# Optimization experiments

Hardware: AMD Instinct MI355X
Metric: run time of the kernel (lower is better)

Reference implementation:

```python
import jax, jax.numpy as jnp
import numpy as np

HIDDEN_SIZE = 1024
NUM_EXPERTS = 8
MOE_INTERMEDIATE_SIZE = 1408
NUM_EXPERTS_PER_TOK = 2
SHARED_EXPERT_INTERMEDIATE_SIZE = 2816
B, T = 2, 1024
W_SCALE = 0.02  # keep pre-activations in a sane range


def setup_inputs() -> dict:
    key = jax.random.key(0)
    ks = jax.random.split(key, 8)
    H, E, I, SI = HIDDEN_SIZE, NUM_EXPERTS, MOE_INTERMEDIATE_SIZE, SHARED_EXPERT_INTERMEDIATE_SIZE
    return {
        "x": jax.random.normal(ks[0], (B, T, H), jnp.float32),
        "gate_w": jax.random.normal(ks[1], (E, H), jnp.float32) * W_SCALE,
        "experts_gate_up": jax.random.normal(ks[2], (E, 2 * I, H), jnp.float32) * W_SCALE,
        "experts_down": jax.random.normal(ks[3], (E, H, I), jnp.float32) * W_SCALE,
        "shared_gate_w": jax.random.normal(ks[4], (SI, H), jnp.float32) * W_SCALE,
        "shared_up_w": jax.random.normal(ks[5], (SI, H), jnp.float32) * W_SCALE,
        "shared_down_w": jax.random.normal(ks[6], (H, SI), jnp.float32) * W_SCALE,
        "shared_expert_gate_w": jax.random.normal(ks[7], (1, H), jnp.float32) * W_SCALE,
    }


def reference(x, gate_w, experts_gate_up, experts_down,
              shared_gate_w, shared_up_w, shared_down_w, shared_expert_gate_w):
    Bx, Tx, H = x.shape
    E = gate_w.shape[0]
    I = experts_down.shape[2]
    x_flat = x.reshape(Bx * Tx, H)            # [N,H]

    # router
    logits = x_flat @ gate_w.T                # [N,E]
    scores = jax.nn.softmax(logits, axis=-1)  # [N,E]
    _, topk_ids = jax.lax.top_k(scores, NUM_EXPERTS_PER_TOK)  # [N,K]
    # NOTE: original normalizes topk_scores but never uses them; combine weight
    # is the RAW softmax score, zeroed for non-selected experts.
    in_topk = jax.nn.one_hot(topk_ids, E, dtype=x.dtype).sum(axis=1)  # [N,E] in {0,1}
    w = scores * in_topk                      # [N,E]

    # dense dispatch over all experts (combine weight zeros out non-routed)
    gu = jnp.einsum('nh,eih->nei', x_flat, experts_gate_up)  # [N,E,2I]
    g, u = gu[..., :I], gu[..., I:]
    h = jax.nn.silu(g) * u                    # [N,E,I]
    expert_out = jnp.einsum('nei,ehi->neh', h, experts_down)  # [N,E,H]
    out = jnp.einsum('neh,ne->nh', expert_out, w)              # [N,H]

    # shared expert (SwiGLU) with sigmoid gate
    shared = (jax.nn.silu(x_flat @ shared_gate_w.T) * (x_flat @ shared_up_w.T)) @ shared_down_w.T
    shared_weight = jax.nn.sigmoid(x_flat @ shared_expert_gate_w.T)  # [N,1]
    out = out + shared_weight * shared
    return out.reshape(Bx, Tx, H)
```

## Files before the change

### kernel.cpp

```cpp
#include <hip/hip_runtime.h>
#include <hip/hip_bf16.h>

#define H_DIM 1024
#define NE 8
#define IDIM 1408
#define SIDIM 2816
#define NTOK 2048

typedef __attribute__((ext_vector_type(8))) _Float16 half8;
typedef __attribute__((ext_vector_type(4))) float f32x4;

__global__ __launch_bounds__(256) void cvt_kernel(const float* __restrict__ src,
                                                  _Float16* __restrict__ dst) {
    size_t i = ((size_t)blockIdx.x * 256 + threadIdx.x) * 8;
    float4 a = *(const float4*)(src + i);
    float4 b = *(const float4*)(src + i + 4);
    half8 o;
    o[0] = (_Float16)a.x; o[1] = (_Float16)a.y; o[2] = (_Float16)a.z; o[3] = (_Float16)a.w;
    o[4] = (_Float16)b.x; o[5] = (_Float16)b.y; o[6] = (_Float16)b.z; o[7] = (_Float16)b.w;
    *(half8*)(dst + i) = o;
}

__global__ __launch_bounds__(256) void router_kernel(
    const float* __restrict__ x, const float* __restrict__ gate_w,
    const float* __restrict__ seg_w, float* __restrict__ wbuf,
    float* __restrict__ swbuf) {
    const int wave = threadIdx.x >> 6, lane = threadIdx.x & 63;
    const int n = blockIdx.x * 4 + wave;
    const float* xr = x + (size_t)n * H_DIM;
    float4 xv[4];
#pragma unroll
    for (int i = 0; i < 4; ++i) xv[i] = *(const float4*)(xr + i * 256 + lane * 4);
    float logits[9];
    for (int e = 0; e < 9; ++e) {
        const float* wr = (e < 8) ? (gate_w + (size_t)e * H_DIM) : seg_w;
        float p = 0.f;
#pragma unroll
        for (int i = 0; i < 4; ++i) {
            float4 wv = *(const float4*)(wr + i * 256 + lane * 4);
            p += xv[i].x * wv.x + xv[i].y * wv.y + xv[i].z * wv.z + xv[i].w * wv.w;
        }
#pragma unroll
        for (int m = 32; m > 0; m >>= 1) p += __shfl_xor(p, m, 64);
        logits[e] = p;
    }
    float mx = logits[0];
#pragma unroll
    for (int e = 1; e < 8; ++e) mx = fmaxf(mx, logits[e]);
    float pe[8], s = 0.f;
#pragma unroll
    for (int e = 0; e < 8; ++e) { pe[e] = expf(logits[e] - mx); s += pe[e]; }
    int i1 = 0;
#pragma unroll
    for (int e = 1; e < 8; ++e) if (logits[e] > logits[i1]) i1 = e;
    int i2 = -1;
#pragma unroll
    for (int e = 0; e < 8; ++e) {
        if (e == i1) continue;
        if (i2 < 0 || logits[e] > logits[i2]) i2 = e;
    }
    if (lane < 8) wbuf[n * NE + lane] = (lane == i1 || lane == i2) ? pe[lane] / s : 0.f;
    if (lane == 8) swbuf[n] = 1.f / (1.f + expf(-logits[8]));
}

__global__ __launch_bounds__(512) void build_lists_kernel(
    const float* __restrict__ wbuf, int* __restrict__ list, int* __restrict__ cnt) {
    const int e = threadIdx.x >> 6, lane = threadIdx.x & 63;
    int base = 0;
    for (int n0 = 0; n0 < NTOK; n0 += 64) {
        float v = wbuf[(size_t)(n0 + lane) * NE + e];
        unsigned long long m = __ballot(v > 0.f);
        int pre = __popcll(m & ((1ull << lane) - 1ull));
        if (v > 0.f) list[e * NTOK + base + pre] = n0 + lane;
        base += __popcll(m);
    }
    if (lane == 0) cnt[e] = base;
}

template <int MODE>
__global__ __launch_bounds__(256) void gemm1_kernel(
    const _Float16* __restrict__ xb, const _Float16* __restrict__ Bg0,
    const _Float16* __restrict__ Bu0, const float* __restrict__ scale,
    const int* __restrict__ list, const int* __restrict__ cnt,
    _Float16* __restrict__ hout) {
    const int e = blockIdx.z;
    const int n0 = blockIdx.x * 64;
    const int m0 = blockIdx.y * 128;
    int count;
    const _Float16 *Bg, *Bu;
    _Float16* out;
    int outStride;
    if (MODE == 0) {
        count = cnt[e];
        if (m0 >= count) return;
        Bg = Bg0 + (size_t)e * (2 * IDIM * H_DIM) + (size_t)n0 * H_DIM;
        Bu = Bg + (size_t)IDIM * H_DIM;
        out = hout + (size_t)e * NTOK * IDIM;
        outStride = IDIM;
    } else {
        count = NTOK;
        Bg = Bg0 + (size_t)n0 * H_DIM;
        Bu = Bu0 + (size_t)n0 * H_DIM;
        out = hout;
        outStride = SIDIM;
    }
    __shared__ __align__(16) _Float16 As[128 * 64];
    __shared__ __align__(16) _Float16 Bgs[64 * 64];
    __shared__ __align__(16) _Float16 Bus[64 * 64];
    __shared__ int toks[128];
    const int tid = threadIdx.x;
    if (tid < 128) {
        int slot = m0 + tid;
        toks[tid] = (MODE == 0) ? list[e * NTOK + (slot < count ? slot : count - 1)] : slot;
    }
    __syncthreads();
    const int lane = tid & 63, wv = tid >> 6;
    const int wr = wv >> 1, wc = wv & 1;
    const int fr = lane & 15, fk = (lane >> 4) * 8;
    f32x4 accg[4][2] = {};
    f32x4 accu[4][2] = {};
    for (int k0 = 0; k0 < H_DIM; k0 += 64) {
#pragma unroll
        for (int it = 0; it < 4; ++it) {
            int c = it * 256 + tid;
            int row = c >> 3, col = (c & 7) << 3;
            *(half8*)&As[row * 64 + col] =
                *(const half8*)(xb + (size_t)toks[row] * H_DIM + k0 + col);
        }
#pragma unroll
        for (int it = 0; it < 2; ++it) {
            int c = it * 256 + tid;
            int row = c >> 3, col = (c & 7) << 3;
            *(half8*)&Bgs[row * 64 + col] = *(const half8*)(Bg + (size_t)row * H_DIM + k0 + col);
            *(half8*)&Bus[row * 64 + col] = *(const half8*)(Bu + (size_t)row * H_DIM + k0 + col);
        }
        __syncthreads();
#pragma unroll
        for (int kk = 0; kk < 2; ++kk) {
            half8 af[4], bgf[2], buf2[2];
#pragma unroll
            for (int mi = 0; mi < 4; ++mi)
                af[mi] = *(const half8*)&As[(wr * 64 + mi * 16 + fr) * 64 + kk * 32 + fk];
#pragma unroll
            for (int ni = 0; ni < 2; ++ni) {
                bgf[ni] = *(const half8*)&Bgs[(wc * 32 + ni * 16 + fr) * 64 + kk * 32 + fk];
                buf2[ni] = *(const half8*)&Bus[(wc * 32 + ni * 16 + fr) * 64 + kk * 32 + fk];
            }
#pragma unroll
            for (int mi = 0; mi < 4; ++mi)
#pragma unroll
                for (int ni = 0; ni < 2; ++ni) {
                    accg[mi][ni] = __builtin_amdgcn_mfma_f32_16x16x32_f16(af[mi], bgf[ni],
                                                                          accg[mi][ni], 0, 0, 0);
                    accu[mi][ni] = __builtin_amdgcn_mfma_f32_16x16x32_f16(af[mi], buf2[ni],
                                                                          accu[mi][ni], 0, 0, 0);
                }
        }
        __syncthreads();
    }
    const int j4 = (lane >> 4) * 4;
#pragma unroll
    for (int mi = 0; mi < 4; ++mi) {
#pragma unroll
        for (int j = 0; j < 4; ++j) {
            int r = wr * 64 + mi * 16 + j4 + j;
            int slot = m0 + r;
            float sc;
            if (MODE == 0)
                sc = (slot < count) ? scale[(size_t)toks[r] * NE + e] : 0.f;
            else
                sc = scale[slot];
#pragma unroll
            for (int ni = 0; ni < 2; ++ni) {
                float g = accg[mi][ni][j];
                float u = accu[mi][ni][j];
                float hv = sc * (g / (1.f + expf(-g))) * u;
                out[(size_t)slot * outStride + n0 + wc * 32 + ni * 16 + fr] = (_Float16)hv;
            }
        }
    }
}

__global__ __launch_bounds__(256) void gemm2_shared_kernel(
    const _Float16* __restrict__ hs, const _Float16* __restrict__ sd_b,
    float* __restrict__ out) {
    const int n0 = blockIdx.x * 64;
    const int m0 = blockIdx.y * 64;
    __shared__ __align__(16) _Float16 As[64 * 64];
    __shared__ __align__(16) _Float16 Bs[64 * 64];
    const int tid = threadIdx.x;
    const int lane = tid & 63, wv = tid >> 6;
    const int wr = wv >> 1, wc = wv & 1;
    const int fr = lane & 15, fk = (lane >> 4) * 8;
    f32x4 acc[2][2] = {};
    for (int k0 = 0; k0 < SIDIM; k0 += 64) {
#pragma unroll
        for (int it = 0; it < 2; ++it) {
            int c = it * 256 + tid;
            int row = c >> 3, col = (c & 7) << 3;
            *(half8*)&As[row * 64 + col] =
                *(const half8*)(hs + (size_t)(m0 + row) * SIDIM + k0 + col);
            *(half8*)&Bs[row * 64 + col] =
                *(const half8*)(sd_b + (size_t)(n0 + row) * SIDIM + k0 + col);
        }
        __syncthreads();
#pragma unroll
        for (int kk = 0; kk < 2; ++kk) {
            half8 af[2], bf[2];
#pragma unroll
            for (int mi = 0; mi < 2; ++mi)
                af[mi] = *(const half8*)&As[(wr * 32 + mi * 16 + fr) * 64 + kk * 32 + fk];
#pragma unroll
            for (int ni = 0; ni < 2; ++ni)
                bf[ni] = *(const half8*)&Bs[(wc * 32 + ni * 16 + fr) * 64 + kk * 32 + fk];
#pragma unroll
            for (int mi = 0; mi < 2; ++mi)
#pragma unroll
                for (int ni = 0; ni < 2; ++ni)
                    acc[mi][ni] = __builtin_amdgcn_mfma_f32_16x16x32_f16(af[mi], bf[ni],
                                                                         acc[mi][ni], 0, 0, 0);
        }
        __syncthreads();
    }
    const int j4 = (lane >> 4) * 4;
#pragma unroll
    for (int mi = 0; mi < 2; ++mi)
#pragma unroll
        for (int j = 0; j < 4; ++j) {
            int r = wr * 32 + mi * 16 + j4 + j;
#pragma unroll
            for (int ni = 0; ni < 2; ++ni)
                out[(size_t)(m0 + r) * H_DIM + n0 + wc * 32 + ni * 16 + fr] = acc[mi][ni][j];
        }
}

__global__ __launch_bounds__(256) void gemm2_moe_kernel(
    const _Float16* __restrict__ hm, const _Float16* __restrict__ down_b,
    const int* __restrict__ list, const int* __restrict__ cnt,
    float* __restrict__ out) {
    const int e = blockIdx.z;
    const int count = cnt[e];
    const int n0 = blockIdx.x * 64;
    const int m0 = blockIdx.y * 64;
    if (m0 >= count) return;
    const _Float16* A = hm + (size_t)e * NTOK * IDIM;
    const _Float16* B = down_b + (size_t)e * H_DIM * IDIM;
    __shared__ __align__(16) _Float16 As[64 * 64];
    __shared__ __align__(16) _Float16 Bs[64 * 64];
    const int tid = threadIdx.x;
    const int lane = tid & 63, wv = tid >> 6;
    const int wr = wv >> 1, wc = wv & 1;
    const int fr = lane & 15, fk = (lane >> 4) * 8;
    f32x4 acc[2][2] = {};
    for (int k0 = 0; k0 < IDIM; k0 += 64) {
#pragma unroll
        for (int it = 0; it < 2; ++it) {
            int c = it * 256 + tid;
            int row = c >> 3, col = (c & 7) << 3;
            *(half8*)&As[row * 64 + col] =
                *(const half8*)(A + (size_t)(m0 + row) * IDIM + k0 + col);
            *(half8*)&Bs[row * 64 + col] =
                *(const half8*)(B + (size_t)(n0 + row) * IDIM + k0 + col);
        }
        __syncthreads();
#pragma unroll
        for (int kk = 0; kk < 2; ++kk) {
            half8 af[2], bf[2];
#pragma unroll
            for (int mi = 0; mi < 2; ++mi)
                af[mi] = *(const half8*)&As[(wr * 32 + mi * 16 + fr) * 64 + kk * 32 + fk];
#pragma unroll
            for (int ni = 0; ni < 2; ++ni)
                bf[ni] = *(const half8*)&Bs[(wc * 32 + ni * 16 + fr) * 64 + kk * 32 + fk];
#pragma unroll
            for (int mi = 0; mi < 2; ++mi)
#pragma unroll
                for (int ni = 0; ni < 2; ++ni)
                    acc[mi][ni] = __builtin_amdgcn_mfma_f32_16x16x32_f16(af[mi], bf[ni],
                                                                         acc[mi][ni], 0, 0, 0);
        }
        __syncthreads();
    }
    const int j4 = (lane >> 4) * 4;
#pragma unroll
    for (int mi = 0; mi < 2; ++mi)
#pragma unroll
        for (int j = 0; j < 4; ++j) {
            int r = wr * 32 + mi * 16 + j4 + j;
            int slot = m0 + r;
            if (slot < count) {
                int tok = list[e * NTOK + slot];
#pragma unroll
                for (int ni = 0; ni < 2; ++ni)
                    atomicAdd(&out[(size_t)tok * H_DIM + n0 + wc * 32 + ni * 16 + fr],
                              acc[mi][ni][j]);
            }
        }
}

extern "C" void kernel_launch(void* const* d_in, const int* in_sizes, int n_in,
                              void* d_out, int out_size, void* d_ws, size_t ws_size,
                              hipStream_t stream) {
    const float* x = (const float*)d_in[0];
    const float* gate_w = (const float*)d_in[1];
    const float* egu = (const float*)d_in[2];
    const float* edown = (const float*)d_in[3];
    const float* sgw = (const float*)d_in[4];
    const float* suw = (const float*)d_in[5];
    const float* sdw = (const float*)d_in[6];
    const float* segw = (const float*)d_in[7];
    float* out = (float*)d_out;

    _Float16* xb = (_Float16*)d_ws;
    _Float16* gu_b = xb + (size_t)NTOK * H_DIM;
    _Float16* down_b = gu_b + (size_t)NE * 2 * IDIM * H_DIM;
    _Float16* sg_b = down_b + (size_t)NE * H_DIM * IDIM;
    _Float16* su_b = sg_b + (size_t)SIDIM * H_DIM;
    _Float16* sd_b = su_b + (size_t)SIDIM * H_DIM;
    _Float16* hm = sd_b + (size_t)H_DIM * SIDIM;
    _Float16* hs = hm + (size_t)NE * NTOK * IDIM;
    float* wbuf = (float*)(hs + (size_t)NTOK * SIDIM);
    float* swbuf = wbuf + NTOK * NE;
    int* cnt = (int*)(swbuf + NTOK);
    int* list = cnt + NE;

    dim3 blk(256);
    cvt_kernel<<<(NTOK * H_DIM) / 2048, blk, 0, stream>>>(x, xb);
    cvt_kernel<<<(NE * 2 * IDIM * H_DIM) / 2048, blk, 0, stream>>>(egu, gu_b);
    cvt_kernel<<<(NE * H_DIM * IDIM) / 2048, blk, 0, stream>>>(edown, down_b);
    cvt_kernel<<<(SIDIM * H_DIM) / 2048, blk, 0, stream>>>(sgw, sg_b);
    cvt_kernel<<<(SIDIM * H_DIM) / 2048, blk, 0, stream>>>(suw, su_b);
    cvt_kernel<<<(H_DIM * SIDIM) / 2048, blk, 0, stream>>>(sdw, sd_b);
    router_kernel<<<NTOK / 4, blk, 0, stream>>>(x, gate_w, segw, wbuf, swbuf);
    build_lists_kernel<<<1, 512, 0, stream>>>(wbuf, list, cnt);
    gemm1_kernel<0><<<dim3(IDIM / 64, NTOK / 128, NE), blk, 0, stream>>>(
        xb, gu_b, nullptr, wbuf, list, cnt, hm);
    gemm1_kernel<1><<<dim3(SIDIM / 64, NTOK / 128, 1), blk, 0, stream>>>(
        xb, sg_b, su_b, swbuf, list, cnt, hs);
    gemm2_shared_kernel<<<dim3(H_DIM / 64, NTOK / 64), blk, 0, stream>>>(hs, sd_b, out);
    gemm2_moe_kernel<<<dim3(H_DIM / 64, NTOK / 64, NE), blk, 0, stream>>>(
        hm, down_b, list, cnt, out);
    (void)in_sizes; (void)n_in; (void)out_size; (void)ws_size;
}
```

Measured before the change: 482.9 us.

## Use direct global-to-LDS loads, merge conversion kernels, enlarge gemm2 tiles

Replaces the register-staged global-to-shared copies in the GEMMs with global_load_lds direct-to-LDS transfers. Merges the six fp32-to-fp16 conversion launches into one kernel, and swaps the grid axes so blocks sharing a weight column tile launch together. Unifies the two down-projection GEMMs into one templated kernel with 128x128 tiles, which raises data reuse but gives fewer blocks and more accumulator registers per thread. The direct-LDS writes rely on the wave-chunk layout lining up with the MFMA fragment reads.

```diff
diff --git a/kernel.cpp b/kernel.cpp
--- a/kernel.cpp
+++ b/kernel.cpp
@@ -10,15 +10,46 @@
 typedef __attribute__((ext_vector_type(8))) _Float16 half8;
 typedef __attribute__((ext_vector_type(4))) float f32x4;
 
-__global__ __launch_bounds__(256) void cvt_kernel(const float* __restrict__ src,
-                                                  _Float16* __restrict__ dst) {
-    size_t i = ((size_t)blockIdx.x * 256 + threadIdx.x) * 8;
-    float4 a = *(const float4*)(src + i);
-    float4 b = *(const float4*)(src + i + 4);
+__device__ __forceinline__ void gload_lds16(const void* g, void* l) {
+    __builtin_amdgcn_global_load_lds(
+        (const __attribute__((address_space(1))) void*)g,
+        (__attribute__((address_space(3))) void*)l, 16, 0, 0);
+}
+
+template <int ROWS>
+__device__ __forceinline__ void stage_rows(const _Float16* __restrict__ src,
+                                           size_t stride, _Float16* lds, int tid) {
+    const int w = tid >> 6, l = tid & 63;
+    const int r8 = l >> 3, c8 = (l & 7) * 8;
+#pragma unroll
+    for (int c = 0; c < ROWS / 8; c += 4) {
+        const int ch = c + w;
+        gload_lds16(src + (size_t)(ch * 8 + r8) * stride + c8, lds + ch * 512);
+    }
+}
+
+__global__ __launch_bounds__(256) void cvt_all_kernel(
+    const float* __restrict__ x, const float* __restrict__ gu,
+    const float* __restrict__ down, const float* __restrict__ sg,
+    const float* __restrict__ su, const float* __restrict__ sd,
+    _Float16* __restrict__ xb, _Float16* __restrict__ gub,
+    _Float16* __restrict__ downb, _Float16* __restrict__ sgb,
+    _Float16* __restrict__ sub, _Float16* __restrict__ sdb) {
+    int b = blockIdx.x;
+    const float* s; _Float16* d; int off;
+    if (b < 1024)       { s = x;    d = xb;    off = b; }
+    else if (b < 12288) { s = gu;   d = gub;   off = b - 1024; }
+    else if (b < 17920) { s = down; d = downb; off = b - 12288; }
+    else if (b < 19328) { s = sg;   d = sgb;   off = b - 17920; }
+    else if (b < 20736) { s = su;   d = sub;   off = b - 19328; }
+    else                { s = sd;   d = sdb;   off = b - 20736; }
+    size_t i = ((size_t)off * 256 + threadIdx.x) * 8;
+    float4 a = *(const float4*)(s + i);
+    float4 c = *(const float4*)(s + i + 4);
     half8 o;
     o[0] = (_Float16)a.x; o[1] = (_Float16)a.y; o[2] = (_Float16)a.z; o[3] = (_Float16)a.w;
-    o[4] = (_Float16)b.x; o[5] = (_Float16)b.y; o[6] = (_Float16)b.z; o[7] = (_Float16)b.w;
-    *(half8*)(dst + i) = o;
+    o[4] = (_Float16)c.x; o[5] = (_Float16)c.y; o[6] = (_Float16)c.z; o[7] = (_Float16)c.w;
+    *(half8*)(d + i) = o;
 }
 
 __global__ __launch_bounds__(256) void router_kernel(
@@ -84,8 +115,8 @@
     const int* __restrict__ list, const int* __restrict__ cnt,
     _Float16* __restrict__ hout) {
     const int e = blockIdx.z;
-    const int n0 = blockIdx.x * 64;
-    const int m0 = blockIdx.y * 128;
+    const int m0 = blockIdx.x * 128;
+    const int n0 = blockIdx.y * 64;
     int count;
     const _Float16 *Bg, *Bu;
     _Float16* out;
@@ -117,23 +148,19 @@
     const int lane = tid & 63, wv = tid >> 6;
     const int wr = wv >> 1, wc = wv & 1;
     const int fr = lane & 15, fk = (lane >> 4) * 8;
+    const int r8 = lane >> 3, c8 = (lane & 7) * 8;
+    const _Float16* aptr[4];
+#pragma unroll
+    for (int c = 0; c < 4; ++c)
+        aptr[c] = xb + (size_t)toks[(c * 4 + wv) * 8 + r8] * H_DIM + c8;
     f32x4 accg[4][2] = {};
     f32x4 accu[4][2] = {};
     for (int k0 = 0; k0 < H_DIM; k0 += 64) {
 #pragma unroll
-        for (int it = 0; it < 4; ++it) {
-            int c = it * 256 + tid;
-            int row = c >> 3, col = (c & 7) << 3;
-            *(half8*)&As[row * 64 + col] =
-                *(const half8*)(xb + (size_t)toks[row] * H_DIM + k0 + col);
-        }
-#pragma unroll
-        for (int it = 0; it < 2; ++it) {
-            int c = it * 256 + tid;
-            int row = c >> 3, col = (c & 7) << 3;
-            *(half8*)&Bgs[row * 64 + col] = *(const half8*)(Bg + (size_t)row * H_DIM + k0 + col);
-            *(half8*)&Bus[row * 64 + col] = *(const half8*)(Bu + (size_t)row * H_DIM + k0 + col);
-        }
+        for (int c = 0; c < 4; ++c)
+            gload_lds16(aptr[c] + k0, As + (c * 4 + wv) * 512);
+        stage_rows<64>(Bg + k0, H_DIM, Bgs, tid);
+        stage_rows<64>(Bu + k0, H_DIM, Bus, tid);
         __syncthreads();
 #pragma unroll
         for (int kk = 0; kk < 2; ++kk) {
@@ -181,42 +208,47 @@
     }
 }
 
-__global__ __launch_bounds__(256) void gemm2_shared_kernel(
-    const _Float16* __restrict__ hs, const _Float16* __restrict__ sd_b,
+template <int MODE>
+__global__ __launch_bounds__(256) void gemm2_kernel(
+    const _Float16* __restrict__ A0, const _Float16* __restrict__ B0,
+    const int* __restrict__ list, const int* __restrict__ cnt,
     float* __restrict__ out) {
-    const int n0 = blockIdx.x * 64;
-    const int m0 = blockIdx.y * 64;
-    __shared__ __align__(16) _Float16 As[64 * 64];
-    __shared__ __align__(16) _Float16 Bs[64 * 64];
+    const int e = blockIdx.z;
+    const int m0 = blockIdx.x * 128;
+    const int n0 = blockIdx.y * 128;
+    constexpr int K = (MODE == 0) ? IDIM : SIDIM;
+    const int count = (MODE == 0) ? cnt[e] : NTOK;
+    if (MODE == 0 && m0 >= count) return;
+    const _Float16* A = (MODE == 0)
+        ? A0 + (size_t)e * NTOK * IDIM + (size_t)m0 * K
+        : A0 + (size_t)m0 * K;
+    const _Float16* B = (MODE == 0)
+        ? B0 + (size_t)e * H_DIM * IDIM + (size_t)n0 * K
+        : B0 + (size_t)n0 * K;
+    __shared__ __align__(16) _Float16 As[128 * 64];
+    __shared__ __align__(16) _Float16 Bs[128 * 64];
     const int tid = threadIdx.x;
     const int lane = tid & 63, wv = tid >> 6;
     const int wr = wv >> 1, wc = wv & 1;
     const int fr = lane & 15, fk = (lane >> 4) * 8;
-    f32x4 acc[2][2] = {};
-    for (int k0 = 0; k0 < SIDIM; k0 += 64) {
-#pragma unroll
-        for (int it = 0; it < 2; ++it) {
-            int c = it * 256 + tid;
-            int row = c >> 3, col = (c & 7) << 3;
-            *(half8*)&As[row * 64 + col] =
-                *(const half8*)(hs + (size_t)(m0 + row) * SIDIM + k0 + col);
-            *(half8*)&Bs[row * 64 + col] =
-                *(const half8*)(sd_b + (size_t)(n0 + row) * SIDIM + k0 + col);
-        }
+    f32x4 acc[4][4] = {};
+    for (int k0 = 0; k0 < K; k0 += 64) {
+        stage_rows<128>(A + k0, K, As, tid);
+        stage_rows<128>(B + k0, K, Bs, tid);
         __syncthreads();
 #pragma unroll
         for (int kk = 0; kk < 2; ++kk) {
-            half8 af[2], bf[2];
-#pragma unroll
-            for (int mi = 0; mi < 2; ++mi)
-                af[mi] = *(const half8*)&As[(wr * 32 + mi * 16 + fr) * 64 + kk * 32 + fk];
-#pragma unroll
-            for (int ni = 0; ni < 2; ++ni)
-                bf[ni] = *(const half8*)&Bs[(wc * 32 + ni * 16 + fr) * 64 + kk * 32 + fk];
-#pragma unroll
-            for (int mi = 0; mi < 2; ++mi)
-#pragma unroll
-                for (int ni = 0; ni < 2; ++ni)
+            half8 af[4], bf[4];
+#pragma unroll
+            for (int mi = 0; mi < 4; ++mi)
+                af[mi] = *(const half8*)&As[(wr * 64 + mi * 16 + fr) * 64 + kk * 32 + fk];
+#pragma unroll
+            for (int ni = 0; ni < 4; ++ni)
+                bf[ni] = *(const half8*)&Bs[(wc * 64 + ni * 16 + fr) * 64 + kk * 32 + fk];
+#pragma unroll
+            for (int mi = 0; mi < 4; ++mi)
+#pragma unroll
+                for (int ni = 0; ni < 4; ++ni)
                     acc[mi][ni] = __builtin_amdgcn_mfma_f32_16x16x32_f16(af[mi], bf[ni],
                                                                          acc[mi][ni], 0, 0, 0);
         }
@@ -224,76 +256,23 @@
     }
     const int j4 = (lane >> 4) * 4;
 #pragma unroll
-    for (int mi = 0; mi < 2; ++mi)
+    for (int mi = 0; mi < 4; ++mi)
 #pragma unroll
         for (int j = 0; j < 4; ++j) {
-            int r = wr * 32 + mi * 16 + j4 + j;
-#pragma unroll
-            for (int ni = 0; ni < 2; ++ni)
-                out[(size_t)(m0 + r) * H_DIM + n0 + wc * 32 + ni * 16 + fr] = acc[mi][ni][j];
-        }
-}
-
-__global__ __launch_bounds__(256) void gemm2_moe_kernel(
-    const _Float16* __restrict__ hm, const _Float16* __restrict__ down_b,
-    const int* __restrict__ list, const int* __restrict__ cnt,
-    float* __restrict__ out) {
-    const int e = blockIdx.z;
-    const int count = cnt[e];
-    const int n0 = blockIdx.x * 64;
-    const int m0 = blockIdx.y * 64;
-    if (m0 >= count) return;
-    const _Float16* A = hm + (size_t)e * NTOK * IDIM;
-    const _Float16* B = down_b + (size_t)e * H_DIM * IDIM;
-    __shared__ __align__(16) _Float16 As[64 * 64];
-    __shared__ __align__(16) _Float16 Bs[64 * 64];
-    const int tid = threadIdx.x;
-    const int lane = tid & 63, wv = tid >> 6;
-    const int wr = wv >> 1, wc = wv & 1;
-    const int fr = lane & 15, fk = (lane >> 4) * 8;
-    f32x4 acc[2][2] = {};
-    for (int k0 = 0; k0 < IDIM; k0 += 64) {
-#pragma unroll
-        for (int it = 0; it < 2; ++it) {
-            int c = it * 256 + tid;
-            int row = c >> 3, col = (c & 7) << 3;
-            *(half8*)&As[row * 64 + col] =
-                *(const half8*)(A + (size_t)(m0 + row) * IDIM + k0 + col);
-            *(half8*)&Bs[row * 64 + col] =
-                *(const half8*)(B + (size_t)(n0 + row) * IDIM + k0 + col);
-        }
-        __syncthreads();
-#pragma unroll
-        for (int kk = 0; kk < 2; ++kk) {
-            half8 af[2], bf[2];
-#pragma unroll
-            for (int mi = 0; mi < 2; ++mi)
-                af[mi] = *(const half8*)&As[(wr * 32 + mi * 16 + fr) * 64 + kk * 32 + fk];
-#pragma unroll
-            for (int ni = 0; ni < 2; ++ni)
-                bf[ni] = *(const half8*)&Bs[(wc * 32 + ni * 16 + fr) * 64 + kk * 32 + fk];
-#pragma unroll
-            for (int mi = 0; mi < 2; ++mi)
-#pragma unroll
-                for (int ni = 0; ni < 2; ++ni)
-                    acc[mi][ni] = __builtin_amdgcn_mfma_f32_16x16x32_f16(af[mi], bf[ni],
-                                                                         acc[mi][ni], 0, 0, 0);
-        }
-        __syncthreads();
-    }
-    const int j4 = (lane >> 4) * 4;
-#pragma unroll
-    for (int mi = 0; mi < 2; ++mi)
-#pragma unroll
-        for (int j = 0; j < 4; ++j) {
-            int r = wr * 32 + mi * 16 + j4 + j;
+            int r = wr * 64 + mi * 16 + j4 + j;
             int slot = m0 + r;
-            if (slot < count) {
-                int tok = list[e * NTOK + slot];
-#pragma unroll
-                for (int ni = 0; ni < 2; ++ni)
-                    atomicAdd(&out[(size_t)tok * H_DIM + n0 + wc * 32 + ni * 16 + fr],
-                              acc[mi][ni][j]);
+            if (MODE == 0) {
+                if (slot < count) {
+                    int tok = list[e * NTOK + slot];
+#pragma unroll
+                    for (int ni = 0; ni < 4; ++ni)
+                        atomicAdd(&out[(size_t)tok * H_DIM + n0 + wc * 64 + ni * 16 + fr],
+                                  acc[mi][ni][j]);
+                }
+            } else {
+#pragma unroll
+                for (int ni = 0; ni < 4; ++ni)
+                    out[(size_t)slot * H_DIM + n0 + wc * 64 + ni * 16 + fr] = acc[mi][ni][j];
             }
         }
 }
@@ -325,20 +304,17 @@
     int* list = cnt + NE;
 
     dim3 blk(256);
-    cvt_kernel<<<(NTOK * H_DIM) / 2048, blk, 0, stream>>>(x, xb);
-    cvt_kernel<<<(NE * 2 * IDIM * H_DIM) / 2048, blk, 0, stream>>>(egu, gu_b);
-    cvt_kernel<<<(NE * H_DIM * IDIM) / 2048, blk, 0, stream>>>(edown, down_b);
-    cvt_kernel<<<(SIDIM * H_DIM) / 2048, blk, 0, stream>>>(sgw, sg_b);
-    cvt_kernel<<<(SIDIM * H_DIM) / 2048, blk, 0, stream>>>(suw, su_b);
-    cvt_kernel<<<(H_DIM * SIDIM) / 2048, blk, 0, stream>>>(sdw, sd_b);
+    cvt_all_kernel<<<22144, blk, 0, stream>>>(x, egu, edown, sgw, suw, sdw,
+                                              xb, gu_b, down_b, sg_b, su_b, sd_b);
     router_kernel<<<NTOK / 4, blk, 0, stream>>>(x, gate_w, segw, wbuf, swbuf);
     build_lists_kernel<<<1, 512, 0, stream>>>(wbuf, list, cnt);
-    gemm1_kernel<0><<<dim3(IDIM / 64, NTOK / 128, NE), blk, 0, stream>>>(
+    gemm1_kernel<0><<<dim3(NTOK / 128, IDIM / 64, NE), blk, 0, stream>>>(
         xb, gu_b, nullptr, wbuf, list, cnt, hm);
-    gemm1_kernel<1><<<dim3(SIDIM / 64, NTOK / 128, 1), blk, 0, stream>>>(
+    gemm1_kernel<1><<<dim3(NTOK / 128, SIDIM / 64, 1), blk, 0, stream>>>(
         xb, sg_b, su_b, swbuf, list, cnt, hs);
-    gemm2_shared_kernel<<<dim3(H_DIM / 64, NTOK / 64), blk, 0, stream>>>(hs, sd_b, out);
-    gemm2_moe_kernel<<<dim3(H_DIM / 64, NTOK / 64, NE), blk, 0, stream>>>(
+    gemm2_kernel<1><<<dim3(NTOK / 128, H_DIM / 128, 1), blk, 0, stream>>>(
+        hs, sd_b, list, cnt, out);
+    gemm2_kernel<0><<<dim3(NTOK / 128, H_DIM / 128, NE), blk, 0, stream>>>(
         hm, down_b, list, cnt, out);
     (void)in_sizes; (void)n_in; (void)out_size; (void)ws_size;
 }
```

After: 592.4 us. 1.23x slower.
